# Performance work log

Measured on AMD Instinct MI355X. Metric: run time of the kernel, lower is better.

The kernel has to match this reference:

```python
import jax, jax.numpy as jnp
import numpy as np

EMBED_DIM = 1024
NUM_HEADS = 16
HEAD_DIM = EMBED_DIM // NUM_HEADS


def setup_inputs() -> dict:
    key = jax.random.key(0)
    ks = jax.random.split(key, 9)
    s = 1.0 / np.sqrt(EMBED_DIM)
    x = jax.random.normal(ks[0], (4, 2048, EMBED_DIM), dtype=jnp.float32)
    # torch.nn.Linear weights are [out_features, in_features]
    Wq = jax.random.uniform(ks[1], (EMBED_DIM, EMBED_DIM), jnp.float32, -s, s)
    bq = jax.random.uniform(ks[2], (EMBED_DIM,), jnp.float32, -s, s)
    Wk = jax.random.uniform(ks[3], (EMBED_DIM, EMBED_DIM), jnp.float32, -s, s)
    bk = jax.random.uniform(ks[4], (EMBED_DIM,), jnp.float32, -s, s)
    Wv = jax.random.uniform(ks[5], (EMBED_DIM, EMBED_DIM), jnp.float32, -s, s)
    bv = jax.random.uniform(ks[6], (EMBED_DIM,), jnp.float32, -s, s)
    Wo = jax.random.uniform(ks[7], (EMBED_DIM, EMBED_DIM), jnp.float32, -s, s)
    bo = jax.random.uniform(ks[8], (EMBED_DIM,), jnp.float32, -s, s)
    return {"x": x, "Wq": Wq, "bq": bq, "Wk": Wk, "bk": bk,
            "Wv": Wv, "bv": bv, "Wo": Wo, "bo": bo}


def reference(x, Wq, bq, Wk, bk, Wv, bv, Wo, bo):
    B, S, E = x.shape
    H, D = NUM_HEADS, HEAD_DIM

    def proj(W, b):
        y = jnp.einsum('bse,fe->bsf', x, W) + b          # Linear: x @ W.T + b
        return y.reshape(B, S, H, D).transpose(0, 2, 1, 3)  # [B,H,S,D]

    q = proj(Wq, bq)
    k = proj(Wk, bk)
    v = proj(Wv, bv)

    scores = jnp.einsum('bhqd,bhkd->bhqk', q, k) / jnp.sqrt(jnp.float32(D))
    attn = jax.nn.soft_sign(scores)                      # softsign, no normalization
    # dropout p=0.0 -> identity
    ctx = jnp.einsum('bhqk,bhkd->bhqd', attn, v)         # [B,H,S,D]
    ctx = ctx.transpose(0, 2, 1, 3).reshape(B, S, E)
    out = jnp.einsum('bse,fe->bsf', ctx, Wo) + bo
    return (out,)
```

## Files before the change

kernel.cpp:

```cpp
#include <hip/hip_runtime.h>
#include <hip/hip_bf16.h>
#include <stdint.h>

#define Bb 4
#define SEQ 2048
#define Ee 1024
#define Hh 16
#define Dh 64
#define Mm (Bb*SEQ)

typedef __attribute__((ext_vector_type(8))) short bfrag;
typedef __attribute__((ext_vector_type(4))) float f32x4;
typedef __attribute__((ext_vector_type(16))) float f32x16;
typedef __attribute__((ext_vector_type(4))) unsigned u32x4;
typedef unsigned short u16;

__device__ __forceinline__ u16 f2bf(float x) {
  __hip_bfloat16 h = __float2bfloat16(x);
  return *reinterpret_cast<u16*>(&h);
}

__device__ __forceinline__ void gll16(const void* g, void* l) {
  __builtin_amdgcn_global_load_lds(
      (const __attribute__((address_space(1))) void*)g,
      (__attribute__((address_space(3))) void*)l, 16, 0, 0);
}

__global__ __launch_bounds__(256) void cast_all(
    const float* __restrict__ x,  const float* __restrict__ wq,
    const float* __restrict__ wk, const float* __restrict__ wv,
    const float* __restrict__ wo,
    u16* __restrict__ xb, u16* __restrict__ wqb, u16* __restrict__ wkb,
    u16* __restrict__ wvb, u16* __restrict__ wob)
{
  int idx = blockIdx.x * 256 + threadIdx.x;
  const float* src; u16* dst; int off;
  if (idx < 2097152) { src = x; dst = xb; off = idx; }
  else {
    int t = idx - 2097152;
    int seg = t >> 18;
    off = t & 262143;
    src = (seg == 0) ? wq : (seg == 1) ? wk : (seg == 2) ? wv : wo;
    dst = (seg == 0) ? wqb : (seg == 1) ? wkb : (seg == 2) ? wvb : wob;
  }
  float4 v = reinterpret_cast<const float4*>(src)[off];
  ushort4 o;
  o.x = f2bf(v.x); o.y = f2bf(v.y); o.z = f2bf(v.z); o.w = f2bf(v.w);
  reinterpret_cast<ushort4*>(dst)[off] = o;
}

template<int OUTMODE>
__global__ __launch_bounds__(256) void gemm_bt(
    const u16* __restrict__ A,
    const u16* __restrict__ W0, const u16* __restrict__ W1, const u16* __restrict__ W2,
    const float* __restrict__ b0, const float* __restrict__ b1, const float* __restrict__ b2,
    void* __restrict__ outp, u16* __restrict__ vt, int K, int N)
{
  __shared__ __align__(16) u16 smem[32768];
  const int tid  = threadIdx.x;
  const int lane = tid & 63;
  const int wid  = tid >> 6;
  const int bm = blockIdx.x * 128;
  const int bn = blockIdx.y * 128;
  const int z  = blockIdx.z;
  const u16*  Wp = (z == 0) ? W0 : (z == 1) ? W1 : W2;
  const float* bp = (z == 0) ? b0 : (z == 1) ? b1 : b2;
  const int wr = (wid >> 1) * 64, wc = (wid & 1) * 64;
  const int lr = lane & 15, lk = (lane >> 4) * 8;
  const int kx = (lr & 7) << 3;

  size_t aoff[4], boff[4];
#pragma unroll
  for (int p = 0; p < 4; ++p) {
    int flat = p * 2048 + tid * 8;
    int r = flat >> 6, c = flat & 63;
    int cs = c ^ ((r & 7) << 3);
    aoff[p] = (size_t)(bm + r) * K + cs;
    boff[p] = (size_t)(bn + r) * K + cs;
  }

  f32x4 acc[4][4] = {};

  auto stage = [&](int kt, int s) {
    u16* As = smem + s * 16384;
    u16* Bs = As + 8192;
#pragma unroll
    for (int p = 0; p < 4; ++p)
      gll16(A + aoff[p] + kt, As + p * 2048 + tid * 8);
#pragma unroll
    for (int p = 0; p < 4; ++p)
      gll16(Wp + boff[p] + kt, Bs + p * 2048 + tid * 8);
  };

  const int NT = K >> 6;
  stage(0, 0);
  __syncthreads();
  for (int t = 0; t < NT; ++t) {
    const int cur = t & 1;
    if (t + 1 < NT) stage((t + 1) << 6, cur ^ 1);
    const u16* As = smem + cur * 16384;
    const u16* Bs = As + 8192;
#pragma unroll
    for (int kk = 0; kk < 2; ++kk) {
      bfrag a[4], b[4];
      const int col = (kk * 32 + lk) ^ kx;
#pragma unroll
      for (int i = 0; i < 4; ++i)
        a[i] = *reinterpret_cast<const bfrag*>(&As[(wr + i * 16 + lr) * 64 + col]);
#pragma unroll
      for (int j = 0; j < 4; ++j)
        b[j] = *reinterpret_cast<const bfrag*>(&Bs[(wc + j * 16 + lr) * 64 + col]);
      __builtin_amdgcn_s_setprio(1);
#pragma unroll
      for (int i = 0; i < 4; ++i)
#pragma unroll
        for (int j = 0; j < 4; ++j)
          acc[i][j] = __builtin_amdgcn_mfma_f32_16x16x32_bf16(a[i], b[j], acc[i][j], 0, 0, 0);
      __builtin_amdgcn_s_setprio(0);
    }
    __syncthreads();
  }

  float bias[4];
#pragma unroll
  for (int j = 0; j < 4; ++j) bias[j] = bp[bn + wc + j * 16 + (lane & 15)];

  if (OUTMODE == 0) {
    const float scl = (z == 0) ? 0.125f : 1.0f;
    u16* cst = smem;
#pragma unroll
    for (int i = 0; i < 4; ++i)
#pragma unroll
      for (int j = 0; j < 4; ++j)
#pragma unroll
        for (int e = 0; e < 4; ++e) {
          int row = wr + i * 16 + (lane >> 4) * 4 + e;
          int c2  = wc + j * 16 + (lane & 15);
          cst[row * 128 + (c2 ^ ((row & 7) << 3))] = f2bf((acc[i][j][e] + bias[j]) * scl);
        }
    __syncthreads();
    if (z < 2) {
      u16* outb = (u16*)outp + (size_t)z * (size_t)Mm * Ee;
#pragma unroll
      for (int p = 0; p < 8; ++p) {
        int chunk = p * 256 + tid;
        int r = chunk >> 4;
        int c = (chunk & 15) * 8;
        int m = bm + r, f = bn + c;
        u16* dst = outb + ((((size_t)(m >> 11) * Hh + (f >> 6)) * SEQ + (m & 2047)) * Dh + (f & 63));
        *reinterpret_cast<bfrag*>(dst) =
            *reinterpret_cast<const bfrag*>(&cst[r * 128 + (c ^ ((r & 7) << 3))]);
      }
    } else {
      const int bq = bm >> 11;
      const int s_base = bm & 2047;
#pragma unroll
      for (int p = 0; p < 8; ++p) {
        int chunk = p * 256 + tid;
        int d = chunk >> 4, sc = chunk & 15;
        int f = bn + d;
        int h = f >> 6, dl = f & 63;
        bfrag o;
#pragma unroll
        for (int e = 0; e < 8; ++e) {
          int sp = sc * 8 + e;
          int ss = (sp & ~12) | ((sp & 4) << 1) | ((sp & 8) >> 1);
          o[e] = (short)cst[ss * 128 + (d ^ ((ss & 7) << 3))];
        }
        *reinterpret_cast<bfrag*>(
            &vt[((size_t)((bq * Hh + h) * Dh + dl)) * SEQ + s_base + sc * 8]) = o;
      }
    }
  } else {
    float* outf = (float*)outp;
    float* cf = reinterpret_cast<float*>(smem);
#pragma unroll
    for (int half = 0; half < 2; ++half) {
      __syncthreads();
      if ((wid >> 1) == half) {
#pragma unroll
        for (int i = 0; i < 4; ++i)
#pragma unroll
          for (int j = 0; j < 4; ++j)
#pragma unroll
            for (int e = 0; e < 4; ++e)
              cf[(i * 16 + (lane >> 4) * 4 + e) * 128 + wc + j * 16 + (lane & 15)] =
                  acc[i][j][e] + bias[j];
      }
      __syncthreads();
#pragma unroll
      for (int p = 0; p < 8; ++p) {
        int chunk = p * 256 + tid;
        int r = chunk >> 5;
        int c = (chunk & 31) * 4;
        *reinterpret_cast<float4*>(&outf[(size_t)(bm + half * 64 + r) * N + bn + c]) =
            *reinterpret_cast<const float4*>(&cf[r * 128 + c]);
      }
    }
  }
}

__global__ __launch_bounds__(256, 4) void attn_kernel(
    const u16* __restrict__ qg_, const u16* __restrict__ kg,
    const u16* __restrict__ vtg, u16* __restrict__ ctx)
{
  __shared__ __align__(16) u16 smem[16384];
  const int tid  = threadIdx.x;
  const int lane = tid & 63;
  const int wid  = tid >> 6;
  const int ql = lane & 31;
  const int hi = lane >> 5;

  const int orig = blockIdx.x;
  const int swz  = (orig & 7) * 128 + (orig >> 3);
  const int bh = swz >> 4;
  const int q0 = (swz & 15) * 128;

  const u16* qb  = qg_ + (size_t)bh * SEQ * Dh;
  const u16* kb  = kg  + (size_t)bh * SEQ * Dh;
  const u16* vtb = vtg + (size_t)bh * Dh * SEQ;

  bfrag qf[4];
#pragma unroll
  for (int db = 0; db < 4; ++db)
    qf[db] = *reinterpret_cast<const bfrag*>(
        &qb[(size_t)(q0 + wid * 32 + ql) * Dh + db * 16 + hi * 8]);

  int koff[2], voff[2];
#pragma unroll
  for (int p = 0; p < 2; ++p) {
    int f = p * 2048 + tid * 8;
    int lrow = f >> 7;
    int log7 = (f & 127) ^ ((lrow & 15) << 3);
    int r = lrow * 2 + (log7 >> 6);
    int c = log7 & 63;
    koff[p] = r * 64 + c;
    voff[p] = r * SEQ + c;
  }

  f32x16 o[2] = {};

  auto stage = [&](int kt, int buf) {
#pragma unroll
    for (int p = 0; p < 2; ++p)
      gll16(kb + (size_t)kt * 64 + koff[p], smem + buf * 4096 + p * 2048 + tid * 8);
#pragma unroll
    for (int p = 0; p < 2; ++p)
      gll16(vtb + kt + voff[p], smem + 8192 + buf * 4096 + p * 2048 + tid * 8);
  };

  stage(0, 0);
  __syncthreads();

  for (int ti = 0; ti < 32; ++ti) {
    const int cur = ti & 1;
    if (ti < 31) stage((ti + 1) * 64, cur ^ 1);
    const u16* Kb = smem + cur * 4096;
    const u16* Vb = smem + 8192 + cur * 4096;

#pragma unroll
    for (int kh = 0; kh < 2; ++kh) {
      f32x16 s = {};
      __builtin_amdgcn_s_setprio(1);
#pragma unroll
      for (int db = 0; db < 4; ++db) {
        const int krow = kh * 32 + ql;
        const int lr2 = krow >> 1;
        const int log7 = ((krow & 1) << 6) | (db * 16 + hi * 8);
        bfrag ka = *reinterpret_cast<const bfrag*>(
            &Kb[lr2 * 128 + (log7 ^ ((lr2 & 15) << 3))]);
        s = __builtin_amdgcn_mfma_f32_32x32x16_bf16(ka, qf[db], s, 0, 0, 0);
      }
      __builtin_amdgcn_s_setprio(0);

      unsigned pw[8];
#pragma unroll
      for (int r = 0; r < 8; ++r) {
        float a = s[2 * r], b = s[2 * r + 1];
        float pa_ = a * __builtin_amdgcn_rcpf(1.0f + __builtin_fabsf(a));
        float pb_ = b * __builtin_amdgcn_rcpf(1.0f + __builtin_fabsf(b));
        pw[r] = __builtin_amdgcn_perm(__builtin_bit_cast(unsigned, pb_),
                                      __builtin_bit_cast(unsigned, pa_),
                                      0x07060302u);
      }
      u32x4 w0 = {pw[0], pw[1], pw[2], pw[3]};
      u32x4 w1 = {pw[4], pw[5], pw[6], pw[7]};
      bfrag pa0 = __builtin_bit_cast(bfrag, w0);
      bfrag pa1 = __builtin_bit_cast(bfrag, w1);

      __builtin_amdgcn_s_setprio(1);
#pragma unroll
      for (int tt = 0; tt < 2; ++tt)
#pragma unroll
        for (int dh = 0; dh < 2; ++dh) {
          const int vrow = dh * 32 + ql;
          const int lr2 = vrow >> 1;
          const int log7 = ((vrow & 1) << 6) | (kh * 32 + tt * 16 + hi * 8);
          bfrag vb = *reinterpret_cast<const bfrag*>(
              &Vb[lr2 * 128 + (log7 ^ ((lr2 & 15) << 3))]);
          o[dh] = __builtin_amdgcn_mfma_f32_32x32x16_bf16(tt ? pa1 : pa0, vb, o[dh], 0, 0, 0);
        }
      __builtin_amdgcn_s_setprio(0);
    }
    __syncthreads();
  }

  u16* cst = smem;
#pragma unroll
  for (int dh = 0; dh < 2; ++dh)
#pragma unroll
    for (int r = 0; r < 16; ++r) {
      int qrow = wid * 32 + (r & 3) + 8 * (r >> 2) + 4 * hi;
      cst[qrow * 64 + dh * 32 + ql] = f2bf(o[dh][r]);
    }
  __syncthreads();
  const int b = bh >> 4, h = bh & 15;
#pragma unroll
  for (int p = 0; p < 4; ++p) {
    int chunk = p * 256 + tid;
    int r = chunk >> 3, cc = (chunk & 7) * 8;
    u16* dst = ctx + ((size_t)(b * SEQ + q0 + r) * Ee + h * Dh + cc);
    *reinterpret_cast<bfrag*>(dst) = *reinterpret_cast<const bfrag*>(&cst[r * 64 + cc]);
  }
}

extern "C" void kernel_launch(void* const* d_in, const int* in_sizes, int n_in,
                              void* d_out, int out_size, void* d_ws, size_t ws_size,
                              hipStream_t stream)
{
  const float* x  = (const float*)d_in[0];
  const float* Wq = (const float*)d_in[1];
  const float* bq = (const float*)d_in[2];
  const float* Wk = (const float*)d_in[3];
  const float* bk = (const float*)d_in[4];
  const float* Wv = (const float*)d_in[5];
  const float* bv = (const float*)d_in[6];
  const float* Wo = (const float*)d_in[7];
  const float* bo = (const float*)d_in[8];
  float* out = (float*)d_out;

  u16* ws  = (u16*)d_ws;
  u16* xb  = ws;
  u16* wqb = ws + 8388608;
  u16* wkb = wqb + 1048576;
  u16* wvb = wkb + 1048576;
  u16* wob = wvb + 1048576;
  u16* qkv = wob + 1048576;
  u16* q_  = qkv;
  u16* k_  = qkv + 8388608;
  u16* vt  = qkv + 2 * 8388608;
  u16* ctx = xb;

  cast_all<<<12288, 256, 0, stream>>>(x, Wq, Wk, Wv, Wo, xb, wqb, wkb, wvb, wob);

  gemm_bt<0><<<dim3(64, 8, 3), 256, 0, stream>>>(xb, wqb, wkb, wvb, bq, bk, bv,
                                                 qkv, vt, Ee, Ee);
  attn_kernel<<<1024, 256, 0, stream>>>(q_, k_, vt, ctx);
  gemm_bt<1><<<dim3(64, 8, 1), 256, 0, stream>>>(ctx, wob, wob, wob, bo, bo, bo,
                                                 out, nullptr, Ee, Ee);
}
```

Measured before the change: 256.0 us.

## Double per-wave query tile in attention to reuse K/V fragments across two query groups

Each attention block now handles 256 queries instead of 128, with each wave processing two 32-row query groups. Every K and V fragment read from LDS feeds two MFMAs, and half as many blocks restage the same K/V tiles. The cost is roughly double the accumulator and query registers, and the 4-waves-per-SIMD launch bound is dropped, so occupancy may fall. Only 512 blocks remain, which may underfill the GPU's compute units.

```diff
diff --git a/kernel.cpp b/kernel.cpp
--- a/kernel.cpp
+++ b/kernel.cpp
@@ -200,7 +200,7 @@
   }
 }
 
-__global__ __launch_bounds__(256, 4) void attn_kernel(
+__global__ __launch_bounds__(256) void attn_kernel(
     const u16* __restrict__ qg_, const u16* __restrict__ kg,
     const u16* __restrict__ vtg, u16* __restrict__ ctx)
 {
@@ -212,19 +212,21 @@
   const int hi = lane >> 5;
 
   const int orig = blockIdx.x;
-  const int swz  = (orig & 7) * 128 + (orig >> 3);
-  const int bh = swz >> 4;
-  const int q0 = (swz & 15) * 128;
+  const int swz  = (orig & 7) * 64 + (orig >> 3);
+  const int bh = swz >> 3;
+  const int q0 = (swz & 7) * 256;
 
   const u16* qb  = qg_ + (size_t)bh * SEQ * Dh;
   const u16* kb  = kg  + (size_t)bh * SEQ * Dh;
   const u16* vtb = vtg + (size_t)bh * Dh * SEQ;
 
-  bfrag qf[4];
-#pragma unroll
-  for (int db = 0; db < 4; ++db)
-    qf[db] = *reinterpret_cast<const bfrag*>(
-        &qb[(size_t)(q0 + wid * 32 + ql) * Dh + db * 16 + hi * 8]);
+  bfrag qf[2][4];
+#pragma unroll
+  for (int qg2 = 0; qg2 < 2; ++qg2)
+#pragma unroll
+    for (int db = 0; db < 4; ++db)
+      qf[qg2][db] = *reinterpret_cast<const bfrag*>(
+          &qb[(size_t)(q0 + wid * 64 + qg2 * 32 + ql) * Dh + db * 16 + hi * 8]);
 
   int koff[2], voff[2];
 #pragma unroll
@@ -238,7 +240,7 @@
     voff[p] = r * SEQ + c;
   }
 
-  f32x16 o[2] = {};
+  f32x16 o[2][2] = {};
 
   auto stage = [&](int kt, int buf) {
 #pragma unroll
@@ -260,7 +262,7 @@
 
 #pragma unroll
     for (int kh = 0; kh < 2; ++kh) {
-      f32x16 s = {};
+      f32x16 s0 = {}, s1 = {};
       __builtin_amdgcn_s_setprio(1);
 #pragma unroll
       for (int db = 0; db < 4; ++db) {
@@ -269,24 +271,38 @@
         const int log7 = ((krow & 1) << 6) | (db * 16 + hi * 8);
         bfrag ka = *reinterpret_cast<const bfrag*>(
             &Kb[lr2 * 128 + (log7 ^ ((lr2 & 15) << 3))]);
-        s = __builtin_amdgcn_mfma_f32_32x32x16_bf16(ka, qf[db], s, 0, 0, 0);
+        s0 = __builtin_amdgcn_mfma_f32_32x32x16_bf16(ka, qf[0][db], s0, 0, 0, 0);
+        s1 = __builtin_amdgcn_mfma_f32_32x32x16_bf16(ka, qf[1][db], s1, 0, 0, 0);
       }
       __builtin_amdgcn_s_setprio(0);
 
-      unsigned pw[8];
+      unsigned pw0[8], pw1[8];
 #pragma unroll
       for (int r = 0; r < 8; ++r) {
-        float a = s[2 * r], b = s[2 * r + 1];
+        float a = s0[2 * r], b = s0[2 * r + 1];
         float pa_ = a * __builtin_amdgcn_rcpf(1.0f + __builtin_fabsf(a));
         float pb_ = b * __builtin_amdgcn_rcpf(1.0f + __builtin_fabsf(b));
-        pw[r] = __builtin_amdgcn_perm(__builtin_bit_cast(unsigned, pb_),
-                                      __builtin_bit_cast(unsigned, pa_),
-                                      0x07060302u);
-      }
-      u32x4 w0 = {pw[0], pw[1], pw[2], pw[3]};
-      u32x4 w1 = {pw[4], pw[5], pw[6], pw[7]};
-      bfrag pa0 = __builtin_bit_cast(bfrag, w0);
-      bfrag pa1 = __builtin_bit_cast(bfrag, w1);
+        pw0[r] = __builtin_amdgcn_perm(__builtin_bit_cast(unsigned, pb_),
+                                       __builtin_bit_cast(unsigned, pa_),
+                                       0x07060302u);
+      }
+#pragma unroll
+      for (int r = 0; r < 8; ++r) {
+        float a = s1[2 * r], b = s1[2 * r + 1];
+        float pa_ = a * __builtin_amdgcn_rcpf(1.0f + __builtin_fabsf(a));
+        float pb_ = b * __builtin_amdgcn_rcpf(1.0f + __builtin_fabsf(b));
+        pw1[r] = __builtin_amdgcn_perm(__builtin_bit_cast(unsigned, pb_),
+                                       __builtin_bit_cast(unsigned, pa_),
+                                       0x07060302u);
+      }
+      u32x4 w00 = {pw0[0], pw0[1], pw0[2], pw0[3]};
+      u32x4 w01 = {pw0[4], pw0[5], pw0[6], pw0[7]};
+      u32x4 w10 = {pw1[0], pw1[1], pw1[2], pw1[3]};
+      u32x4 w11 = {pw1[4], pw1[5], pw1[6], pw1[7]};
+      bfrag pa00 = __builtin_bit_cast(bfrag, w00);
+      bfrag pa01 = __builtin_bit_cast(bfrag, w01);
+      bfrag pa10 = __builtin_bit_cast(bfrag, w10);
+      bfrag pa11 = __builtin_bit_cast(bfrag, w11);
 
       __builtin_amdgcn_s_setprio(1);
 #pragma unroll
@@ -298,7 +314,8 @@
           const int log7 = ((vrow & 1) << 6) | (kh * 32 + tt * 16 + hi * 8);
           bfrag vb = *reinterpret_cast<const bfrag*>(
               &Vb[lr2 * 128 + (log7 ^ ((lr2 & 15) << 3))]);
-          o[dh] = __builtin_amdgcn_mfma_f32_32x32x16_bf16(tt ? pa1 : pa0, vb, o[dh], 0, 0, 0);
+          o[0][dh] = __builtin_amdgcn_mfma_f32_32x32x16_bf16(tt ? pa01 : pa00, vb, o[0][dh], 0, 0, 0);
+          o[1][dh] = __builtin_amdgcn_mfma_f32_32x32x16_bf16(tt ? pa11 : pa10, vb, o[1][dh], 0, 0, 0);
         }
       __builtin_amdgcn_s_setprio(0);
     }
@@ -307,16 +324,18 @@
 
   u16* cst = smem;
 #pragma unroll
-  for (int dh = 0; dh < 2; ++dh)
-#pragma unroll
-    for (int r = 0; r < 16; ++r) {
-      int qrow = wid * 32 + (r & 3) + 8 * (r >> 2) + 4 * hi;
-      cst[qrow * 64 + dh * 32 + ql] = f2bf(o[dh][r]);
-    }
+  for (int qg2 = 0; qg2 < 2; ++qg2)
+#pragma unroll
+    for (int dh = 0; dh < 2; ++dh)
+#pragma unroll
+      for (int r = 0; r < 16; ++r) {
+        int qrow = wid * 64 + qg2 * 32 + (r & 3) + 8 * (r >> 2) + 4 * hi;
+        cst[qrow * 64 + dh * 32 + ql] = f2bf(o[qg2][dh][r]);
+      }
   __syncthreads();
   const int b = bh >> 4, h = bh & 15;
 #pragma unroll
-  for (int p = 0; p < 4; ++p) {
+  for (int p = 0; p < 8; ++p) {
     int chunk = p * 256 + tid;
     int r = chunk >> 3, cc = (chunk & 7) * 8;
     u16* dst = ctx + ((size_t)(b * SEQ + q0 + r) * Ee + h * Dh + cc);
@@ -355,7 +374,7 @@
 
   gemm_bt<0><<<dim3(64, 8, 3), 256, 0, stream>>>(xb, wqb, wkb, wvb, bq, bk, bv,
                                                  qkv, vt, Ee, Ee);
-  attn_kernel<<<1024, 256, 0, stream>>>(q_, k_, vt, ctx);
+  attn_kernel<<<512, 256, 0, stream>>>(q_, k_, vt, ctx);
   gemm_bt<1><<<dim3(64, 8, 1), 256, 0, stream>>>(ctx, wob, wob, wob, bo, bo, bo,
                                                  out, nullptr, Ee, Ee);
 }
```

Measured after the change: 259.5 us. About the same (+1.4%).
